# Kernel tuning notes

Measured on AMD Instinct MI355X. Metric: run time of the kernel, lower is better.

Reference implementation:

```python
import jax, jax.numpy as jnp
import numpy as np
from jax import lax

K = 1024          # number_embeddings
D = 256           # embedding_dimension
BETA = 0.25


def setup_inputs() -> dict:
    key = jax.random.key(0)
    k1, k2 = jax.random.split(key)
    z = jax.random.normal(k1, (32, 32, 32, D), dtype=jnp.float32)
    # codebook initialized uniform in [-1/K, 1/K] as in the original layer
    codebook = jax.random.uniform(k2, (K, D), dtype=jnp.float32,
                                  minval=-1.0 / K, maxval=1.0 / K)
    return {"z": z, "codebook": codebook}


def reference(z, codebook):
    # z: [B, H, W, D] -> flatten to [N, D]
    zf = z.reshape(-1, D)
    # squared-distance matrix [N, K]: ||z||^2 + ||e||^2 - 2 z e^T
    d = ((zf * zf).sum(axis=1, keepdims=True)
         + (codebook * codebook).sum(axis=1)[None, :]
         - 2.0 * (zf @ codebook.T))
    idx = jnp.argmin(d, axis=1)                      # [N]
    quantized = codebook[idx].reshape(z.shape)       # gather + reshape

    commitment_loss = BETA * jnp.mean((lax.stop_gradient(quantized) - z) ** 2)
    # straight-through estimator
    quantized_ste = z + lax.stop_gradient(quantized - z)

    # perplexity from empirical code usage (scatter-add instead of NxK one-hot)
    n = zf.shape[0]
    avg_probs = jnp.zeros((K,), dtype=zf.dtype).at[idx].add(1.0) / n
    perplexity = jnp.exp(-jnp.sum(avg_probs * jnp.log(avg_probs + 1e-10)))

    return quantized_ste, idx, jnp.zeros((), dtype=z.dtype), commitment_loss, perplexity
```

## Files before the change

kernel.cpp:

```cpp
#include <hip/hip_runtime.h>

#define N_ROWS 32768
#define DIM 256
#define KCODES 1024

#define Q_N (N_ROWS * DIM)
#define IDX_OFF Q_N
#define ZERO_OFF (Q_N + N_ROWS)
#define LOSS_OFF (ZERO_OFF + 1)
#define PERP_OFF (ZERO_OFF + 2)

#define AMBIG_S  0.12f

#define TC 64
#define NT (KCODES / TC)
#define PAIR_GRID 768
#define FULL_GRID 1024
#define GATHER_BLOCKS 1024
#define GATHER_ITERS 8

typedef __attribute__((ext_vector_type(8))) _Float16 f16x8;
typedef __attribute__((ext_vector_type(4))) float f32x4;
typedef unsigned short u16;
typedef unsigned long long u64;


__device__ inline u16 f16bits(_Float16 h) {
    union { _Float16 h; u16 u; } x; x.h = h; return x.u;
}

__device__ inline bool lexless(float av, int ai, float bv, int bi) {
    return av < bv || (av == bv && ai < bi);
}

typedef __attribute__((address_space(3))) unsigned int as3_uint;
typedef __attribute__((address_space(1))) const unsigned int as1_uint;
__device__ inline void gload_lds16(const void* g, void* l) {
    __builtin_amdgcn_global_load_lds((as1_uint*)g, (as3_uint*)l, 16, 0, 0);
}

__global__ __launch_bounds__(256) void vq_prep_cb(const float* __restrict__ cb,
                                                  float* __restrict__ sen,
                                                  u16* __restrict__ e16,
                                                  unsigned* __restrict__ hist,
                                                  unsigned* __restrict__ pcnt,
                                                  unsigned* __restrict__ fcnt) {
    int b = blockIdx.x, t = threadIdx.x;
    if (b < 4) {
        hist[b * 256 + t] = 0u;
        if (b == 0 && t == 0) { *pcnt = 0u; *fcnt = 0u; }
    }
    int code = b * 4 + (t >> 6);
    int lane = t & 63;
    size_t eoff = (size_t)code * DIM + lane * 4;
    float4 v = *(const float4*)(cb + eoff);
    double s = (double)v.x * v.x + (double)v.y * v.y + (double)v.z * v.z + (double)v.w * v.w;
    #pragma unroll
    for (int off = 32; off; off >>= 1) s += __shfl_down(s, off, 64);
    if (lane == 0) sen[code] = (float)s;
    ushort4 us;
    us.x = f16bits((_Float16)(-1024.0f * v.x));
    us.y = f16bits((_Float16)(-1024.0f * v.y));
    us.z = f16bits((_Float16)(-1024.0f * v.z));
    us.w = f16bits((_Float16)(-1024.0f * v.w));
    *(ushort4*)(e16 + eoff) = us;
}

__global__ __launch_bounds__(256, 2) void vq_mfma(const float* __restrict__ z,
                                                  const u16* __restrict__ e16,
                                                  const float* __restrict__ sen,
                                                  float* __restrict__ idx_out,
                                                  unsigned* __restrict__ pcnt,
                                                  uint2* __restrict__ pairlist,
                                                  unsigned* __restrict__ fcnt,
                                                  unsigned* __restrict__ fulllist,
                                                  u64* __restrict__ fullkey) {
    __shared__ char lds[2][32768];
    const int tid = threadIdx.x;
    const int wid = tid >> 6;
    const int lane = tid & 63;
    const int col16 = lane & 15;
    const int koct = lane >> 4;
    const int s3 = col16 & 7;
    const int rowbase = blockIdx.x * 128 + wid * 32;

    f16x8 zf[2][8];
    #pragma unroll
    for (int g = 0; g < 2; ++g) {
        const float* zp = z + (size_t)(rowbase + g * 16 + col16) * DIM + koct * 8;
        #pragma unroll
        for (int dc = 0; dc < 8; ++dc) {
            float4 f0 = *(const float4*)(zp + dc * 32);
            float4 f1 = *(const float4*)(zp + dc * 32 + 4);
            f16x8 h;
            h[0] = (_Float16)f0.x; h[1] = (_Float16)f0.y;
            h[2] = (_Float16)f0.z; h[3] = (_Float16)f0.w;
            h[4] = (_Float16)f1.x; h[5] = (_Float16)f1.y;
            h[6] = (_Float16)f1.z; h[7] = (_Float16)f1.w;
            zf[g][dc] = h;
        }
    }

    unsigned k1[2][4], k2[2][4], k3[2][4];
    #pragma unroll
    for (int g = 0; g < 2; ++g)
        #pragma unroll
        for (int r = 0; r < 4; ++r) { k1[g][r] = k2[g][r] = k3[g][r] = 0xFFFFFFFFu; }

    auto STAGE = [&](int tt, int b) {
        #pragma unroll
        for (int r = 0; r < 8; ++r) {
            int p = r * 256 + tid;
            int src = p ^ ((p >> 5) & 7);
            const char* sp = (const char*)e16 + (size_t)tt * 32768 + src * 16;
            gload_lds16(sp, &lds[b][p * 16]);
        }
    };

    STAGE(0, 0);
    __syncthreads();

    for (int tt = 0; tt < NT; ++tt) {
        if (tt + 1 < NT) STAGE(tt + 1, (tt + 1) & 1);
        const char* bb = lds[tt & 1];
        f32x4 acc[2][4];
        #pragma unroll
        for (int ct = 0; ct < 4; ++ct) {
            float sv = sen[tt * TC + ct * 16 + col16];
            float b0 = fmaf(512.0f, sv, 512.0f);
            acc[0][ct] = (f32x4){b0, b0, b0, b0};
            acc[1][ct] = (f32x4){b0, b0, b0, b0};
        }
        #pragma unroll
        for (int dc = 0; dc < 8; ++dc) {
            int swcol = ((dc * 4 + koct) ^ s3) * 16;
            #pragma unroll
            for (int ct = 0; ct < 4; ++ct) {
                int off = (ct * 16 + col16) * 512 + swcol;
                f16x8 bv = *(const f16x8*)(bb + off);
                acc[0][ct] = __builtin_amdgcn_mfma_f32_16x16x32_f16(zf[0][dc], bv, acc[0][ct], 0, 0, 0);
                acc[1][ct] = __builtin_amdgcn_mfma_f32_16x16x32_f16(zf[1][dc], bv, acc[1][ct], 0, 0, 0);
            }
        }
        #pragma unroll
        for (int ct = 0; ct < 4; ++ct) {
            const unsigned lidx = (unsigned)(tt * 4 + ct);
            #pragma unroll
            for (int g = 0; g < 2; ++g)
                #pragma unroll
                for (int r = 0; r < 4; ++r) {
                    float s = acc[g][ct][r];
                    unsigned key = (__float_as_uint(s) & 0xFFFFFFC0u) | lidx;
                    unsigned o1 = k1[g][r];
                    k1[g][r] = min(o1, key);
                    k3[g][r] = min(k3[g][r], max(k2[g][r], key));
                    k2[g][r] = min(max(key, o1), k2[g][r]);
                }
        }
        __syncthreads();
    }

    #pragma unroll
    for (int g = 0; g < 2; ++g)
        #pragma unroll
        for (int r = 0; r < 4; ++r) {
            float a1 = __uint_as_float(k1[g][r] & 0xFFFFFFC0u);
            float a2 = __uint_as_float(k2[g][r] & 0xFFFFFFC0u);
            float a3 = __uint_as_float(k3[g][r] & 0xFFFFFFC0u);
            int l1 = (int)(k1[g][r] & 63u), l2 = (int)(k2[g][r] & 63u), l3 = (int)(k3[g][r] & 63u);
            int b1 = (l1 >> 2) * TC + (l1 & 3) * 16 + col16;
            int b2 = (l2 >> 2) * TC + (l2 & 3) * 16 + col16;
            int b3 = (l3 >> 2) * TC + (l3 & 3) * 16 + col16;
            #pragma unroll
            for (int m = 1; m < 16; m <<= 1) {
                float o1 = __shfl_xor(a1, m, 64), o2 = __shfl_xor(a2, m, 64), o3 = __shfl_xor(a3, m, 64);
                int p1 = __shfl_xor(b1, m, 64), p2 = __shfl_xor(b2, m, 64), p3 = __shfl_xor(b3, m, 64);
                #pragma unroll
                for (int k = 0; k < 3; ++k) {
                    float ov = (k == 0) ? o1 : (k == 1) ? o2 : o3;
                    int oi = (k == 0) ? p1 : (k == 1) ? p2 : p3;
                    if (lexless(ov, oi, a1, b1)) {
                        a3 = a2; b3 = b2; a2 = a1; b2 = b1; a1 = ov; b1 = oi;
                    } else if (lexless(ov, oi, a2, b2)) {
                        a3 = a2; b3 = b2; a2 = ov; b2 = oi;
                    } else if (lexless(ov, oi, a3, b3)) {
                        a3 = ov; b3 = oi;
                    }
                }
            }
            if (col16 == 0) {
                int row = rowbase + g * 16 + koct * 4 + r;
                idx_out[row] = (float)b1;
                if (a2 - a1 < AMBIG_S) {
                    if (a3 - a1 < AMBIG_S) {
                        unsigned slot = atomicAdd(fcnt, 1u);
                        fulllist[slot] = (unsigned)row;
                        fullkey[slot] = ~0ull;
                    } else {
                        unsigned slot = atomicAdd(pcnt, 1u);
                        pairlist[slot] = make_uint2((unsigned)row,
                                                    ((unsigned)b1 << 16) | (unsigned)b2);
                    }
                }
            }
        }
}

__device__ inline float szn_wave(const float* __restrict__ zrow, int lane) {
    int sub = lane & 15;
    int hb = sub >> 3;
    int j = sub & 7;
    const float* a = zrow + hb * 128 + j;
    float v0 = a[0];
    float c = __fmul_rn(v0, v0);
    #pragma unroll
    for (int i = 1; i < 16; ++i) {
        float w = a[8 * i];
        c = __fadd_rn(c, __fmul_rn(w, w));
    }
    float p;
    p = __shfl_xor(c, 1, 64); c = __fadd_rn(c, p);
    p = __shfl_xor(c, 2, 64); c = __fadd_rn(c, p);
    p = __shfl_xor(c, 4, 64); c = __fadd_rn(c, p);
    p = __shfl_xor(c, 8, 64); c = __fadd_rn(c, p);
    return c;
}

__global__ __launch_bounds__(256) void vq_fixpair(const float* __restrict__ z,
                                                  const float* __restrict__ cb,
                                                  const float* __restrict__ sen,
                                                  const unsigned* __restrict__ pcnt,
                                                  const uint2* __restrict__ pairlist,
                                                  float* __restrict__ idx_out) {
    int wave = blockIdx.x * 4 + (threadIdx.x >> 6);
    int lane = threadIdx.x & 63;
    int half = lane >> 5, s5 = lane & 31;
    int n = (int)*pcnt;
    for (int w = wave; w < n; w += PAIR_GRID * 4) {
        uint2 pr = pairlist[w];
        int row = (int)pr.x;
        int c1 = (int)(pr.y >> 16), c2 = (int)(pr.y & 0xffffu);
        const float* zrow = z + (size_t)row * DIM;
        float sz = szn_wave(zrow, lane);
        int c = half ? c2 : c1;
        const float* zp = zrow + s5 * 8;
        const float* ep = cb + (size_t)c * DIM + s5 * 8;
        float4 za = *(const float4*)zp, zb = *(const float4*)(zp + 4);
        float4 ea = *(const float4*)ep, eb = *(const float4*)(ep + 4);
        double acc = (double)ea.x * za.x + (double)ea.y * za.y
                   + (double)ea.z * za.z + (double)ea.w * za.w
                   + (double)eb.x * zb.x + (double)eb.y * zb.y
                   + (double)eb.z * zb.z + (double)eb.w * zb.w;
        #pragma unroll
        for (int m = 1; m < 32; m <<= 1) acc += __shfl_xor(acc, m, 64);
        double d2 = __shfl(acc, 32, 64);
        if (lane == 0) {
            float A1 = __fadd_rn(sz, sen[c1]);
            float dref1 = __fmaf_rn(-2.0f, (float)acc, A1);
            float A2 = __fadd_rn(sz, sen[c2]);
            float dref2 = __fmaf_rn(-2.0f, (float)d2, A2);
            int win = lexless(dref1, c1, dref2, c2) ? c1 : c2;
            idx_out[row] = (float)win;
        }
    }
}

__global__ __launch_bounds__(64) void vq_fixfull(const float* __restrict__ z,
                                                 const float* __restrict__ cb,
                                                 const float* __restrict__ sen,
                                                 const unsigned* __restrict__ fcnt,
                                                 const unsigned* __restrict__ fulllist,
                                                 u64* __restrict__ fullkey) {
    __shared__ float et[64 * 257];
    __shared__ float zs[DIM];
    const int t = threadIdx.x;
    unsigned nitems = (*fcnt) * 16u;
    for (unsigned item = blockIdx.x; item < nitems; item += FULL_GRID) {
        int slot = (int)(item >> 4);
        int row = (int)fulllist[slot];
        int c0 = (int)(item & 15u) * 64;
        #pragma unroll 8
        for (int i = 0; i < 64; ++i) {
            int g4 = i * 64 + t;
            int code = g4 >> 6, d0 = (g4 & 63) * 4;
            float4 v = *(const float4*)(cb + (size_t)(c0 + code) * DIM + d0);
            int base = code * 257 + d0;
            et[base] = v.x; et[base + 1] = v.y; et[base + 2] = v.z; et[base + 3] = v.w;
        }
        {
            float4 v = *(const float4*)(z + (size_t)row * DIM + t * 4);
            zs[t * 4] = v.x; zs[t * 4 + 1] = v.y; zs[t * 4 + 2] = v.z; zs[t * 4 + 3] = v.w;
        }
        __syncthreads();
        float sz = szn_wave(zs, t);
        const int rb = t * 257;
        double a0 = 0.0, a1 = 0.0, a2 = 0.0, a3 = 0.0;
        #pragma unroll 16
        for (int d = 0; d < DIM; d += 4) {
            a0 += (double)et[rb + d]     * (double)zs[d];
            a1 += (double)et[rb + d + 1] * (double)zs[d + 1];
            a2 += (double)et[rb + d + 2] * (double)zs[d + 2];
            a3 += (double)et[rb + d + 3] * (double)zs[d + 3];
        }
        double dot = (a0 + a1) + (a2 + a3);
        int c = c0 + t;
        float A = __fadd_rn(sz, sen[c]);
        float dref = __fmaf_rn(-2.0f, (float)dot, A);
        float bv = dref; int bi = c;
        #pragma unroll
        for (int m = 1; m < 64; m <<= 1) {
            float ov = __shfl_xor(bv, m, 64);
            int oi = __shfl_xor(bi, m, 64);
            if (lexless(ov, oi, bv, bi)) { bv = ov; bi = oi; }
        }
        if (t == 0) {
            u64 key = ((u64)__float_as_uint(bv) << 32) | (unsigned)bi;
            atomicMin(&fullkey[slot], key);
        }
        __syncthreads();
    }
}

__global__ __launch_bounds__(256) void vq_resolve(const unsigned* __restrict__ fcnt,
                                                  const unsigned* __restrict__ fulllist,
                                                  const u64* __restrict__ fullkey,
                                                  float* __restrict__ idx_out) {
    int n = (int)*fcnt;
    for (int i = threadIdx.x; i < n; i += 256)
        idx_out[fulllist[i]] = (float)(unsigned)(fullkey[i] & 0xFFFFFFFFu);
}

__global__ __launch_bounds__(256) void vq_gather(const float* __restrict__ z,
                                                 const float* __restrict__ cb,
                                                 const float* __restrict__ idxf,
                                                 float* __restrict__ qout,
                                                 unsigned* __restrict__ hist,
                                                 double* __restrict__ partials) {
    const int tid = threadIdx.x;
    double lacc = 0.0;
    #pragma unroll
    for (int it = 0; it < GATHER_ITERS; ++it) {
        int g = it * (GATHER_BLOCKS * 256) + blockIdx.x * 256 + tid;
        int row = g >> 6, c4 = g & 63;
        int idx = (int)idxf[row];
        if (c4 == 0) atomicAdd(&hist[idx], 1u);
        float4 zv = *(const float4*)(z + (size_t)g * 4);
        float4 qv = *(const float4*)(cb + (size_t)idx * DIM + c4 * 4);
        float dx = qv.x - zv.x, dy = qv.y - zv.y, dz = qv.z - zv.z, dw = qv.w - zv.w;
        float4 o;
        o.x = zv.x + dx; o.y = zv.y + dy; o.z = zv.z + dz; o.w = zv.w + dw;
        *(float4*)(qout + (size_t)g * 4) = o;
        lacc += (double)(dx * dx + dy * dy + dz * dz + dw * dw);
    }
    #pragma unroll
    for (int off = 32; off; off >>= 1) lacc += __shfl_down(lacc, off, 64);
    __shared__ double wsum[4];
    int lane = tid & 63, wv = tid >> 6;
    if (lane == 0) wsum[wv] = lacc;
    __syncthreads();
    if (tid == 0)
        partials[blockIdx.x] = (wsum[0] + wsum[1]) + (wsum[2] + wsum[3]);
}

__global__ __launch_bounds__(1024) void vq_finalize(const unsigned* __restrict__ hist,
                                                    const double* __restrict__ partials,
                                                    float* __restrict__ out) {
    __shared__ float red[1024];
    __shared__ double redd[1024];
    int t = threadIdx.x;
    float p = (float)hist[t] * (1.0f / (float)N_ROWS);
    red[t] = p * logf(p + 1e-10f);
    redd[t] = partials[t];
    __syncthreads();
    for (int s = 512; s; s >>= 1) {
        if (t < s) { red[t] += red[t + s]; redd[t] += redd[t + s]; }
        __syncthreads();
    }
    if (t == 0) {
        out[ZERO_OFF] = 0.0f;
        out[LOSS_OFF] = (float)(0.25 * redd[0] / (double)Q_N);
        out[PERP_OFF] = expf(-red[0]);
    }
}

extern "C" void kernel_launch(void* const* d_in, const int* in_sizes, int n_in,
                              void* d_out, int out_size, void* d_ws, size_t ws_size,
                              hipStream_t stream) {
    const float* z = (const float*)d_in[0];
    const float* cb = (const float*)d_in[1];
    float* out = (float*)d_out;

    float* sen = (float*)d_ws;
    unsigned* hist = (unsigned*)((char*)d_ws + 4096);
    unsigned* pcnt = (unsigned*)((char*)d_ws + 8192);
    unsigned* fcnt = (unsigned*)((char*)d_ws + 8196);
    uint2* pairlist = (uint2*)((char*)d_ws + 8448);
    unsigned* fulllist = (unsigned*)((char*)d_ws + 270592);
    u16* e16 = (u16*)((char*)d_ws + 401664);
    double* partials = (double*)((char*)d_ws + 925952);
    u64* fullkey = (u64*)((char*)d_ws + 934144);

    vq_prep_cb<<<KCODES / 4, 256, 0, stream>>>(cb, sen, e16, hist, pcnt, fcnt);
    vq_mfma<<<N_ROWS / 128, 256, 0, stream>>>(z, e16, sen, out + IDX_OFF,
                                              pcnt, pairlist, fcnt, fulllist, fullkey);
    vq_fixpair<<<PAIR_GRID, 256, 0, stream>>>(z, cb, sen, pcnt, pairlist, out + IDX_OFF);
    vq_fixfull<<<FULL_GRID, 64, 0, stream>>>(z, cb, sen, fcnt, fulllist, fullkey);
    vq_resolve<<<1, 256, 0, stream>>>(fcnt, fulllist, fullkey, out + IDX_OFF);
    vq_gather<<<GATHER_BLOCKS, 256, 0, stream>>>(z, cb, out + IDX_OFF, out, hist, partials);
    vq_finalize<<<1, 1024, 0, stream>>>(hist, partials, out);
}
```

Baseline: 106.4 us.

## Split codebook search across two block halves and merge top-3 candidates

The distance/argmin kernel now launches 512 blocks, each scanning half of the codebook for 128 rows, which doubles the block count from 256 so more of the GPU's compute units are filled. Each half writes its top-3 candidates per row to workspace. A new merge kernel combines the two candidate lists and does the ambiguity classification that previously lived in the main kernel. The cost is reloading and converting z twice, extra global traffic for the candidate buffer, and one more kernel launch.

```diff
diff --git a/kernel.cpp b/kernel.cpp
--- a/kernel.cpp
+++ b/kernel.cpp
@@ -13,7 +13,7 @@
 #define AMBIG_S  0.12f
 
 #define TC 64
-#define NT (KCODES / TC)
+#define HALF_TILES 8
 #define PAIR_GRID 768
 #define FULL_GRID 1024
 #define GATHER_BLOCKS 1024
@@ -69,12 +69,7 @@
 __global__ __launch_bounds__(256, 2) void vq_mfma(const float* __restrict__ z,
                                                   const u16* __restrict__ e16,
                                                   const float* __restrict__ sen,
-                                                  float* __restrict__ idx_out,
-                                                  unsigned* __restrict__ pcnt,
-                                                  uint2* __restrict__ pairlist,
-                                                  unsigned* __restrict__ fcnt,
-                                                  unsigned* __restrict__ fulllist,
-                                                  u64* __restrict__ fullkey) {
+                                                  unsigned* __restrict__ cand) {
     __shared__ char lds[2][32768];
     const int tid = threadIdx.x;
     const int wid = tid >> 6;
@@ -82,7 +77,9 @@
     const int col16 = lane & 15;
     const int koct = lane >> 4;
     const int s3 = col16 & 7;
-    const int rowbase = blockIdx.x * 128 + wid * 32;
+    const int rowblk = blockIdx.x & 255;
+    const int half = blockIdx.x >> 8;
+    const int rowbase = rowblk * 128 + wid * 32;
 
     f16x8 zf[2][8];
     #pragma unroll
@@ -112,7 +109,8 @@
         for (int r = 0; r < 8; ++r) {
             int p = r * 256 + tid;
             int src = p ^ ((p >> 5) & 7);
-            const char* sp = (const char*)e16 + (size_t)tt * 32768 + src * 16;
+            const char* sp = (const char*)e16 + (size_t)half * 262144
+                             + (size_t)tt * 32768 + src * 16;
             gload_lds16(sp, &lds[b][p * 16]);
         }
     };
@@ -120,13 +118,13 @@
     STAGE(0, 0);
     __syncthreads();
 
-    for (int tt = 0; tt < NT; ++tt) {
-        if (tt + 1 < NT) STAGE(tt + 1, (tt + 1) & 1);
+    for (int tt = 0; tt < HALF_TILES; ++tt) {
+        if (tt + 1 < HALF_TILES) STAGE(tt + 1, (tt + 1) & 1);
         const char* bb = lds[tt & 1];
         f32x4 acc[2][4];
         #pragma unroll
         for (int ct = 0; ct < 4; ++ct) {
-            float sv = sen[tt * TC + ct * 16 + col16];
+            float sv = sen[half * 512 + tt * TC + ct * 16 + col16];
             float b0 = fmaf(512.0f, sv, 512.0f);
             acc[0][ct] = (f32x4){b0, b0, b0, b0};
             acc[1][ct] = (f32x4){b0, b0, b0, b0};
@@ -168,9 +166,9 @@
             float a2 = __uint_as_float(k2[g][r] & 0xFFFFFFC0u);
             float a3 = __uint_as_float(k3[g][r] & 0xFFFFFFC0u);
             int l1 = (int)(k1[g][r] & 63u), l2 = (int)(k2[g][r] & 63u), l3 = (int)(k3[g][r] & 63u);
-            int b1 = (l1 >> 2) * TC + (l1 & 3) * 16 + col16;
-            int b2 = (l2 >> 2) * TC + (l2 & 3) * 16 + col16;
-            int b3 = (l3 >> 2) * TC + (l3 & 3) * 16 + col16;
+            int b1 = half * 512 + (l1 >> 2) * TC + (l1 & 3) * 16 + col16;
+            int b2 = half * 512 + (l2 >> 2) * TC + (l2 & 3) * 16 + col16;
+            int b3 = half * 512 + (l3 >> 2) * TC + (l3 & 3) * 16 + col16;
             #pragma unroll
             for (int m = 1; m < 16; m <<= 1) {
                 float o1 = __shfl_xor(a1, m, 64), o2 = __shfl_xor(a2, m, 64), o3 = __shfl_xor(a3, m, 64);
@@ -190,20 +188,52 @@
             }
             if (col16 == 0) {
                 int row = rowbase + g * 16 + koct * 4 + r;
-                idx_out[row] = (float)b1;
-                if (a2 - a1 < AMBIG_S) {
-                    if (a3 - a1 < AMBIG_S) {
-                        unsigned slot = atomicAdd(fcnt, 1u);
-                        fulllist[slot] = (unsigned)row;
-                        fullkey[slot] = ~0ull;
-                    } else {
-                        unsigned slot = atomicAdd(pcnt, 1u);
-                        pairlist[slot] = make_uint2((unsigned)row,
-                                                    ((unsigned)b1 << 16) | (unsigned)b2);
-                    }
-                }
+                unsigned* cp = cand + ((size_t)half * N_ROWS + row) * 6;
+                cp[0] = __float_as_uint(a1); cp[1] = (unsigned)b1;
+                cp[2] = __float_as_uint(a2); cp[3] = (unsigned)b2;
+                cp[4] = __float_as_uint(a3); cp[5] = (unsigned)b3;
             }
         }
+}
+
+__global__ __launch_bounds__(256) void vq_merge(const unsigned* __restrict__ cand,
+                                                float* __restrict__ idx_out,
+                                                unsigned* __restrict__ pcnt,
+                                                uint2* __restrict__ pairlist,
+                                                unsigned* __restrict__ fcnt,
+                                                unsigned* __restrict__ fulllist,
+                                                u64* __restrict__ fullkey) {
+    int row = blockIdx.x * 256 + threadIdx.x;
+    const unsigned* cA = cand + (size_t)row * 6;
+    const unsigned* cB = cand + ((size_t)N_ROWS + row) * 6;
+    float a1 = __uint_as_float(cA[0]), a2 = __uint_as_float(cA[2]), a3 = __uint_as_float(cA[4]);
+    int   b1 = (int)cA[1], b2 = (int)cA[3], b3 = (int)cA[5];
+    float o1 = __uint_as_float(cB[0]), o2 = __uint_as_float(cB[2]), o3 = __uint_as_float(cB[4]);
+    int   p1 = (int)cB[1], p2 = (int)cB[3], p3 = (int)cB[5];
+    #pragma unroll
+    for (int k = 0; k < 3; ++k) {
+        float ov = (k == 0) ? o1 : (k == 1) ? o2 : o3;
+        int oi = (k == 0) ? p1 : (k == 1) ? p2 : p3;
+        if (lexless(ov, oi, a1, b1)) {
+            a3 = a2; b3 = b2; a2 = a1; b2 = b1; a1 = ov; b1 = oi;
+        } else if (lexless(ov, oi, a2, b2)) {
+            a3 = a2; b3 = b2; a2 = ov; b2 = oi;
+        } else if (lexless(ov, oi, a3, b3)) {
+            a3 = ov; b3 = oi;
+        }
+    }
+    idx_out[row] = (float)b1;
+    if (a2 - a1 < AMBIG_S) {
+        if (a3 - a1 < AMBIG_S) {
+            unsigned slot = atomicAdd(fcnt, 1u);
+            fulllist[slot] = (unsigned)row;
+            fullkey[slot] = ~0ull;
+        } else {
+            unsigned slot = atomicAdd(pcnt, 1u);
+            pairlist[slot] = make_uint2((unsigned)row,
+                                        ((unsigned)b1 << 16) | (unsigned)b2);
+        }
+    }
 }
 
 __device__ inline float szn_wave(const float* __restrict__ zrow, int lane) {
@@ -399,10 +429,12 @@
     u16* e16 = (u16*)((char*)d_ws + 401664);
     double* partials = (double*)((char*)d_ws + 925952);
     u64* fullkey = (u64*)((char*)d_ws + 934144);
+    unsigned* cand = (unsigned*)((char*)d_ws + 1196288);
 
     vq_prep_cb<<<KCODES / 4, 256, 0, stream>>>(cb, sen, e16, hist, pcnt, fcnt);
-    vq_mfma<<<N_ROWS / 128, 256, 0, stream>>>(z, e16, sen, out + IDX_OFF,
-                                              pcnt, pairlist, fcnt, fulllist, fullkey);
+    vq_mfma<<<512, 256, 0, stream>>>(z, e16, sen, cand);
+    vq_merge<<<N_ROWS / 256, 256, 0, stream>>>(cand, out + IDX_OFF,
+                                               pcnt, pairlist, fcnt, fulllist, fullkey);
     vq_fixpair<<<PAIR_GRID, 256, 0, stream>>>(z, cb, sen, pcnt, pairlist, out + IDX_OFF);
     vq_fixfull<<<FULL_GRID, 64, 0, stream>>>(z, cb, sen, fcnt, fulllist, fullkey);
     vq_resolve<<<1, 256, 0, stream>>>(fcnt, fulllist, fullkey, out + IDX_OFF);
```

After: 105.8 us. Within noise of the previous version (-0.6%).
